# Kernel tuning notes

Hardware: AMD Instinct MI355X
Metric: run time of the kernel (lower is better)

## Reference

```python
import jax, jax.numpy as jnp
import numpy as np

D_MODEL = 1024
N_HEADS = 16
DH = D_MODEL // N_HEADS
ROPE_THETA = 10000.0


def rotate_half(u):
    h = u.shape[-1] // 2
    return jnp.concatenate([-u[..., h:], u[..., :h]], axis=-1)


def apply_rope(q, k, cos, sin):
    return q * cos + rotate_half(q) * sin, k * cos + rotate_half(k) * sin


def setup_inputs() -> dict:
    key = jax.random.key(0)
    ks = jax.random.split(key, 6)
    B, S = 2, 2048
    x = jax.random.normal(ks[0], (B, S, D_MODEL), dtype=jnp.float32)
    y = jax.random.normal(ks[1], (B, S, D_MODEL), dtype=jnp.float32)
    wq = 0.01 * jax.random.normal(ks[2], (D_MODEL, D_MODEL), dtype=jnp.float32)
    wk = 0.01 * jax.random.normal(ks[3], (D_MODEL, D_MODEL), dtype=jnp.float32)
    wv = 0.01 * jax.random.normal(ks[4], (D_MODEL, D_MODEL), dtype=jnp.float32)
    wo = 0.01 * jax.random.normal(ks[5], (D_MODEL, D_MODEL), dtype=jnp.float32)
    return {"x": x, "y": y, "wq": wq, "wk": wk, "wv": wv, "wo": wo}


def reference(x, y, wq, wk, wv, wo):
    B, S, D = x.shape
    past_length = 0  # default; kv_cache=None

    Q = x @ wq.T                      # (B,S,D)
    K = y                             # NOTE: K is y un-projected (as in source)
    V = y @ wv.T
    # K1 = x @ wk.T is computed in the source but immediately overwritten
    # by the buggy second apply_rope call -> wk is unused in the output.
    V1 = x @ wo.T

    def heads(t):
        return t.reshape(B, S, N_HEADS, DH).transpose(0, 2, 1, 3)  # (B,H,S,dh)

    q_h, k_h, v_h, v1_h = heads(Q), heads(K), heads(V), heads(V1)

    # RoPE tables (past_length:past_length+S rows of the cache)
    freqs = 1.0 / ROPE_THETA ** (jnp.arange(0, DH, 2, dtype=jnp.float32) / DH)
    emb = jnp.arange(past_length, past_length + S, dtype=jnp.float32)[:, None] * freqs[None, :]
    cos = jnp.concatenate([jnp.cos(emb), jnp.cos(emb)], axis=-1)[None, None]  # (1,1,S,dh)
    sin = jnp.concatenate([jnp.sin(emb), jnp.sin(emb)], axis=-1)[None, None]

    q_h, k_h = apply_rope(q_h, k_h, cos, sin)
    # faithful to source: k1 = rope applied AGAIN to the already-roped k
    _, k1_h = apply_rope(q_h, k_h, cos, sin)

    k_full = jnp.concatenate([k_h, k1_h], axis=2)   # (B,H,2S,dh)
    v_full = jnp.concatenate([v_h, v1_h], axis=2)
    S_full = k_full.shape[2]

    # mask: tril(diagonal=past_length) over (S,S_full), last S cols = eye(S)
    rows = jnp.arange(S)[:, None]
    cols = jnp.arange(S_full)[None, :]
    mask = cols <= rows + past_length
    mask = mask.at[:, -S:].set(jnp.eye(S, dtype=bool))  # (S,S_full)

    scores = jnp.einsum("bhqd,bhkd->bhqk", q_h, k_full) / jnp.sqrt(jnp.asarray(DH, x.dtype))
    scores = jnp.where(mask[None, None], scores, jnp.asarray(-1e30, x.dtype))
    attn = jax.nn.softmax(scores, axis=-1)
    out = jnp.einsum("bhqk,bhkd->bhqd", attn, v_full)
    out = out.transpose(0, 2, 1, 3).reshape(B, S, D)

    k_ret = k_full[:, :, :-S, :]
    return out, k_ret
```

## Files before the change

### kernel.cpp

```cpp
#include <hip/hip_runtime.h>

#define DM 1024
#define NHEADS 16
#define DHEAD 64
#define BB 2
#define SS 2048
#define BH (BB*NHEADS)

typedef __attribute__((ext_vector_type(8))) short short8;
typedef __attribute__((ext_vector_type(4))) float float4v;
typedef unsigned short ushort_t;

#define LN1E4_D32 0.28782313662425572f

static __device__ __forceinline__ unsigned short f2bf(float f) {
    union { float f; unsigned u; } v; v.f = f;
    unsigned r = v.u + 0x7fffu + ((v.u >> 16) & 1u);
    return (unsigned short)(r >> 16);
}
static __device__ __forceinline__ float bf2f(unsigned short u) {
    union { float f; unsigned u; } v; v.u = ((unsigned)u) << 16;
    return v.f;
}
static __device__ __forceinline__ unsigned cvtpk_bf16(float lo, float hi) {
    unsigned r;
    asm("v_cvt_pk_bf16_f32 %0, %1, %2" : "=v"(r) : "v"(lo), "v"(hi));
    return r;
}

static __device__ __forceinline__ void gload16(const ushort_t* g, ushort_t* l) {
    __builtin_amdgcn_global_load_lds(
        (const __attribute__((address_space(1))) void*)g,
        (__attribute__((address_space(3))) void*)l, 16, 0, 0);
}

__global__ __launch_bounds__(256) void cvt_tile_kernel(
        const float* __restrict__ x, const float* __restrict__ wq,
        const float* __restrict__ wv, const float* __restrict__ wo,
        ushort_t* __restrict__ xb, ushort_t* __restrict__ wqb,
        ushort_t* __restrict__ wvb, ushort_t* __restrict__ wob) {
    int C = blockIdx.x * 256 + threadIdx.x;
    int c  = C & 511;
    int tl = C >> 9;
    int rb = tl >> 5, kb = tl & 31;
    const float* src; ushort_t* dst; int r0;
    if (rb < 32)      { src = x;  r0 = rb * 128;        dst = xb  + (size_t)tl * 4096; }
    else if (rb < 40) { src = wq; r0 = (rb - 32) * 128; dst = wqb + (size_t)(((rb - 32) * 32) + kb) * 4096; }
    else if (rb < 48) { src = wv; r0 = (rb - 40) * 128; dst = wvb + (size_t)(((rb - 40) * 32) + kb) * 4096; }
    else              { src = wo; r0 = (rb - 48) * 128; dst = wob + (size_t)(((rb - 48) * 32) + kb) * 4096; }
    int row = c >> 2, g = c & 3;
    int kk3 = g ^ ((row >> 1) & 3);
    const float* s = src + (size_t)(r0 + row) * DM + kb * 32 + kk3 * 8;
    float4 a0 = *reinterpret_cast<const float4*>(s);
    float4 a1 = *reinterpret_cast<const float4*>(s + 4);
    short8 v;
    v[0] = (short)f2bf(a0.x); v[1] = (short)f2bf(a0.y);
    v[2] = (short)f2bf(a0.z); v[3] = (short)f2bf(a0.w);
    v[4] = (short)f2bf(a1.x); v[5] = (short)f2bf(a1.y);
    v[6] = (short)f2bf(a1.z); v[7] = (short)f2bf(a1.w);
    *reinterpret_cast<short8*>(dst + c * 8) = v;
}

__global__ __launch_bounds__(256) void rope_k_kernel(const float* __restrict__ y,
        float* __restrict__ kout, ushort_t* __restrict__ khb, ushort_t* __restrict__ yb) {
    int t = blockIdx.x * blockDim.x + threadIdx.x;
    int i8 = t & 3;
    int s  = (t >> 2) & (SS - 1);
    int bh = t >> 13;
    int h = bh & (NHEADS - 1), b = bh >> 4;

    const float* yp = y + ((size_t)(b * SS + s)) * DM + h * DHEAD + i8 * 8;
    float4 a0 = *reinterpret_cast<const float4*>(yp);
    float4 a1 = *reinterpret_cast<const float4*>(yp + 4);
    float4 b0 = *reinterpret_cast<const float4*>(yp + 32);
    float4 b1 = *reinterpret_cast<const float4*>(yp + 36);
    float u0[8] = {a0.x, a0.y, a0.z, a0.w, a1.x, a1.y, a1.z, a1.w};
    float u1[8] = {b0.x, b0.y, b0.z, b0.w, b1.x, b1.y, b1.z, b1.w};
    float lo[8], hi[8];
#pragma unroll
    for (int j = 0; j < 8; j++) {
        int i = i8 * 8 + j;
        float freq = __expf(-(float)i * LN1E4_D32);
        float th = (float)s * freq;
        float cv = cosf(th), sv = sinf(th);
        lo[j] = u0[j] * cv - u1[j] * sv;
        hi[j] = u1[j] * cv + u0[j] * sv;
    }
    float* op = kout + ((size_t)bh * SS + s) * DHEAD + i8 * 8;
    *reinterpret_cast<float4*>(op)      = (float4){lo[0], lo[1], lo[2], lo[3]};
    *reinterpret_cast<float4*>(op + 4)  = (float4){lo[4], lo[5], lo[6], lo[7]};
    *reinterpret_cast<float4*>(op + 32) = (float4){hi[0], hi[1], hi[2], hi[3]};
    *reinterpret_cast<float4*>(op + 36) = (float4){hi[4], hi[5], hi[6], hi[7]};

    ushort_t* kb = khb + ((size_t)bh * 32 + (s >> 6)) * 4096 + (s & 63) * 64;
    short8 vlo, vhi;
#pragma unroll
    for (int j = 0; j < 8; j++) { vlo[j] = (short)f2bf(lo[j]); vhi[j] = (short)f2bf(hi[j]); }
    *reinterpret_cast<short8*>(kb + ((i8 ^ (s & 7)) << 3))       = vlo;
    *reinterpret_cast<short8*>(kb + (((i8 + 4) ^ (s & 7)) << 3)) = vhi;

    int rowm = b * SS + s;
    int rowin = rowm & 127, rbm = rowm >> 7;
    int g = i8 ^ ((rowin >> 1) & 3);
    ushort_t* yt = yb + ((size_t)(rbm * 32 + h * 2)) * 4096 + rowin * 32 + (g << 3);
    short8 ulo, uhi;
#pragma unroll
    for (int j = 0; j < 8; j++) { ulo[j] = (short)f2bf(u0[j]); uhi[j] = (short)f2bf(u1[j]); }
    *reinterpret_cast<short8*>(yt)        = ulo;
    *reinterpret_cast<short8*>(yt + 4096) = uhi;
}

__global__ __launch_bounds__(256, 2) void gemm3_kernel(
        const ushort_t* __restrict__ xb, const ushort_t* __restrict__ yb,
        const ushort_t* __restrict__ wqb, const ushort_t* __restrict__ wvb,
        const ushort_t* __restrict__ wob,
        ushort_t* __restrict__ qh, ushort_t* __restrict__ vt, ushort_t* __restrict__ v1h) {
    __shared__ __align__(16) char smem[34816];
    ushort_t* As = (ushort_t*)smem;
    ushort_t* Bs = (ushort_t*)(smem + 16384);
    ushort_t (*Ct)[136] = (ushort_t(*)[136])smem;

    int bid = blockIdx.x;
    int xcd = bid & 7;
    int s_  = bid >> 3;
    int zo  = s_ >> 5;
    int z   = (zo == 0) ? 0 : (zo == 1 ? 2 : 1);
    int t_  = s_ & 31;
    int n0  = (t_ >> 2) * 128;
    int m0  = (xcd * 4 + (t_ & 3)) * 128;

    const ushort_t* A = (z == 1) ? yb : xb;
    const ushort_t* W = (z == 0) ? wqb : (z == 1 ? wvb : wob);
    ushort_t* O = (z == 0) ? qh : (z == 1 ? vt : v1h);

    const ushort_t* Atl = A + (size_t)(m0 >> 7) * 32 * 4096;
    const ushort_t* Wtl = W + (size_t)(n0 >> 7) * 32 * 4096;

    int tid = threadIdx.x;
    int wave = tid >> 6, lane = tid & 63, quad = lane >> 4, l15 = lane & 15;
    int wr = (wave >> 1) * 64, wc = (wave & 1) * 64;

    int gi0 = tid * 8, gi1 = (256 + tid) * 8;
    int li0 = (tid & 192) * 8, li1 = (256 + (tid & 192)) * 8;

    int aoff[4], boff[4];
#pragma unroll
    for (int mi = 0; mi < 4; mi++) {
        int row = wr + mi * 16 + l15;
        aoff[mi] = row * 32 + ((quad ^ ((row >> 1) & 3)) << 3);
    }
#pragma unroll
    for (int ni = 0; ni < 4; ni++) {
        int row = wc + ni * 16 + l15;
        boff[ni] = row * 32 + ((quad ^ ((row >> 1) & 3)) << 3);
    }

    float4v acc[4][4];
#pragma unroll
    for (int a = 0; a < 4; a++)
#pragma unroll
        for (int b = 0; b < 4; b++)
            acc[a][b] = (float4v){0.f, 0.f, 0.f, 0.f};

    gload16(Atl + gi0, As + li0); gload16(Atl + gi1, As + li1);
    gload16(Wtl + gi0, Bs + li0); gload16(Wtl + gi1, Bs + li1);
    int cur = 0;

    for (int kb = 0; kb < 32; kb++) {
        __syncthreads();
        if (kb + 1 < 32) {
            const ushort_t* at = Atl + (size_t)(kb + 1) * 4096;
            const ushort_t* wt = Wtl + (size_t)(kb + 1) * 4096;
            int nb = (cur ^ 1) * 4096;
            gload16(at + gi0, As + nb + li0); gload16(at + gi1, As + nb + li1);
            gload16(wt + gi0, Bs + nb + li0); gload16(wt + gi1, Bs + nb + li1);
        }
        const ushort_t* Ac = As + cur * 4096;
        const ushort_t* Bc = Bs + cur * 4096;
        short8 af[4], bfr[4];
#pragma unroll
        for (int mi = 0; mi < 4; mi++)
            af[mi] = *reinterpret_cast<const short8*>(&Ac[aoff[mi]]);
#pragma unroll
        for (int ni = 0; ni < 4; ni++)
            bfr[ni] = *reinterpret_cast<const short8*>(&Bc[boff[ni]]);
#pragma unroll
        for (int mi = 0; mi < 4; mi++)
#pragma unroll
            for (int ni = 0; ni < 4; ni++)
                acc[mi][ni] = __builtin_amdgcn_mfma_f32_16x16x32_bf16(af[mi], bfr[ni], acc[mi][ni], 0, 0, 0);
        cur ^= 1;
    }

    if (z == 0) {
#pragma unroll
        for (int mi = 0; mi < 4; mi++)
#pragma unroll
            for (int r = 0; r < 4; r++) {
                int m = m0 + wr + mi * 16 + quad * 4 + r;
                float pos = (float)(m & (SS - 1));
#pragma unroll
                for (int ni = 0; ni < 2; ni++) {
                    int d = ni * 16 + l15;
                    float f = __expf(-(float)d * LN1E4_D32);
                    float th = pos * f;
                    float cv, sv;
                    __sincosf(th, &sv, &cv);
                    float u0 = acc[mi][ni][r], u1 = acc[mi][ni + 2][r];
                    acc[mi][ni][r]     = u0 * cv - u1 * sv;
                    acc[mi][ni + 2][r] = u1 * cv + u0 * sv;
                }
            }
    }

    __syncthreads();
#pragma unroll
    for (int mi = 0; mi < 4; mi++)
#pragma unroll
        for (int ni = 0; ni < 4; ni++) {
            int col = wc + ni * 16 + l15;
#pragma unroll
            for (int r = 0; r < 4; r++)
                Ct[wr + mi * 16 + quad * 4 + r][col] = f2bf(acc[mi][ni][r]);
        }
    __syncthreads();
    int h0 = n0 >> 6;
    if (z == 1) {
        int b = m0 >> 11;
        int s0 = m0 & (SS - 1);
#pragma unroll
        for (int it = 0; it < 8; it++) {
            int c = it * 256 + tid;
            int dh  = c & 63;
            int k16 = (c >> 6) & 15;
            int hh  = c >> 10;
            short8 v;
#pragma unroll
            for (int e = 0; e < 8; e++)
                v[e] = (short)Ct[k16 * 8 + e][hh * 64 + dh];
            int kt = (s0 >> 6) + (k16 >> 3);
            size_t off = ((size_t)((b * NHEADS + h0 + hh) * 32 + kt)) * 4096
                       + dh * 64 + (((k16 & 7) ^ (dh & 7)) << 3);
            *reinterpret_cast<short8*>(&O[off]) = v;
        }
    } else {
#pragma unroll
        for (int it = 0; it < 8; it++) {
            int c = it * 256 + tid;
            int o = c >> 3, j = c & 7;
            int hh = o >> 7, mr = o & 127;
            int m = m0 + mr, b = m >> 11, si = m & (SS - 1);
            uint4 v = *reinterpret_cast<const uint4*>(&Ct[mr][hh * 64 + j * 8]);
            *reinterpret_cast<uint4*>(
                &O[((size_t)((b * NHEADS + h0 + hh) * SS + si)) * DHEAD + j * 8]) = v;
        }
    }
}

template<bool MASKED>
static __device__ __forceinline__ void attn_tile(
        const ushort_t* __restrict__ Kc, const ushort_t* __restrict__ Vc, int kbase,
        int quad, int l15, int q0w, const short8* qf,
        ushort_t* __restrict__ Psw, float4v* Oa, float& lsum) {
    float4v sa[4];
#pragma unroll
    for (int t2 = 0; t2 < 4; t2++) sa[t2] = (float4v){0.f, 0.f, 0.f, 0.f};
#pragma unroll
    for (int t2 = 0; t2 < 4; t2++) {
        int key = t2 * 16 + l15;
        int ro = key * 64, sw = key & 7;
#pragma unroll
        for (int half = 0; half < 2; half++) {
            short8 kf = *reinterpret_cast<const short8*>(&Kc[ro + (((half * 4 + quad) ^ sw) << 3)]);
            sa[t2] = __builtin_amdgcn_mfma_f32_16x16x32_bf16(kf, qf[half], sa[t2], 0, 0, 0);
        }
    }
    int query = q0w + l15;
    int swl = l15 & 7;
#pragma unroll
    for (int t2 = 0; t2 < 4; t2++) {
        float p[4];
#pragma unroll
        for (int r = 0; r < 4; r++) {
            float e = __expf(sa[t2][r] * 0.125f);
            if (MASKED) {
                int key = kbase + t2 * 16 + quad * 4 + r;
                p[r] = (key <= query) ? e : 0.f;
            } else {
                p[r] = e;
            }
        }
        lsum += (p[0] + p[1]) + (p[2] + p[3]);
        unsigned w0 = cvtpk_bf16(p[0], p[1]);
        unsigned w1 = cvtpk_bf16(p[2], p[3]);
        int chunk = (((t2 * 2 + (quad >> 1)) ^ swl) << 3) + (quad & 1) * 4;
        *reinterpret_cast<unsigned*>(&Psw[l15 * 64 + chunk])     = w0;
        *reinterpret_cast<unsigned*>(&Psw[l15 * 64 + chunk + 2]) = w1;
    }
    short8 pf0 = *reinterpret_cast<const short8*>(&Psw[l15 * 64 + ((quad ^ swl) << 3)]);
    short8 pf1 = *reinterpret_cast<const short8*>(&Psw[l15 * 64 + (((4 + quad) ^ swl) << 3)]);
#pragma unroll
    for (int t = 0; t < 4; t++) {
        int dh = t * 16 + l15;
        int ro = dh * 64, sw = dh & 7;
        short8 vf0 = *reinterpret_cast<const short8*>(&Vc[ro + ((quad ^ sw) << 3)]);
        short8 vf1 = *reinterpret_cast<const short8*>(&Vc[ro + (((4 + quad) ^ sw) << 3)]);
        Oa[t] = __builtin_amdgcn_mfma_f32_16x16x32_bf16(pf0, vf0, Oa[t], 0, 0, 0);
        Oa[t] = __builtin_amdgcn_mfma_f32_16x16x32_bf16(pf1, vf1, Oa[t], 0, 0, 0);
    }
}

__global__ __launch_bounds__(512, 2) void attn_kernel(
        const ushort_t* __restrict__ qh, const float* __restrict__ kf32,
        const ushort_t* __restrict__ khb, const ushort_t* __restrict__ vtb,
        const ushort_t* __restrict__ v1h, float* __restrict__ out) {
    __shared__ __align__(16) ushort_t Ks[2][4096];
    __shared__ __align__(16) ushort_t Vt[2][4096];
    __shared__ __align__(16) ushort_t Ps[8][16][64];
    __shared__ float sdiag[8][16];
    __shared__ float sred[8][16];

    int bid = blockIdx.x;
    int bh = (bid & 7) * 4 + ((bid >> 3) & 3);
    int jq = 15 - (bid >> 5);
    int q0 = jq * 128;

    int tid = threadIdx.x, wave = tid >> 6, lane = tid & 63, quad = lane >> 4, l15 = lane & 15;
    int q0w = q0 + wave * 16;
    const ushort_t* qp  = qh  + (size_t)bh * SS * DHEAD;
    const float*    kp  = kf32 + (size_t)bh * SS * DHEAD;
    const ushort_t* v1p = v1h + (size_t)bh * SS * DHEAD;
    const ushort_t* ktb = khb + (size_t)bh * 32 * 4096;
    const ushort_t* vtt = vtb + (size_t)bh * 32 * 4096;

    short8 qf[2];
    qf[0] = *reinterpret_cast<const short8*>(&qp[(q0w + l15) * DHEAD + quad * 8]);
    qf[1] = *reinterpret_cast<const short8*>(&qp[(q0w + l15) * DHEAD + 32 + quad * 8]);

    float4v Oa[4];
#pragma unroll
    for (int t = 0; t < 4; t++) Oa[t] = (float4v){0.f, 0.f, 0.f, 0.f};
    float lsum = 0.f;

    int gi = tid * 8;
    int li = (tid & 448) * 8;

    int ntiles = jq * 2 + 2;
    gload16(ktb + gi, &Ks[0][li]);
    gload16(vtt + gi, &Vt[0][li]);
    int cur = 0;

    for (int kt = 0; kt < ntiles; kt++) {
        __syncthreads();
        if (kt + 1 < ntiles) {
            const ushort_t* gk = ktb + (size_t)(kt + 1) * 4096;
            const ushort_t* gv = vtt + (size_t)(kt + 1) * 4096;
            int nb = cur ^ 1;
            gload16(gk + gi, &Ks[nb][li]);
            gload16(gv + gi, &Vt[nb][li]);
        }
        int kbase = kt * 64;
        if (kbase <= q0w + 15) {
            if (kbase + 63 <= q0w)
                attn_tile<false>(Ks[cur], Vt[cur], kbase, quad, l15, q0w, qf,
                                 &Ps[wave][0][0], Oa, lsum);
            else
                attn_tile<true>(Ks[cur], Vt[cur], kbase, quad, l15, q0w, qf,
                                &Ps[wave][0][0], Oa, lsum);
        }
        cur ^= 1;
    }

    lsum += __shfl_xor(lsum, 16);
    lsum += __shfl_xor(lsum, 32);
    if (quad == 0) sred[wave][l15] = lsum;

    {
        int sk = q0w + l15;
        const float* krow = kp + (size_t)sk * DHEAD;
        short8 k1lo, k1hi;
#pragma unroll
        for (int j = 0; j < 8; j++) {
            int d = quad * 8 + j;
            float f = __expf(-(float)d * LN1E4_D32);
            float th = (float)sk * f;
            float cv, sv;
            __sincosf(th, &sv, &cv);
            float a = krow[d], b2 = krow[d + 32];
            k1lo[j] = (short)f2bf(a * cv - b2 * sv);
            k1hi[j] = (short)f2bf(b2 * cv + a * sv);
        }
        float4v sd4 = (float4v){0.f, 0.f, 0.f, 0.f};
        sd4 = __builtin_amdgcn_mfma_f32_16x16x32_bf16(qf[0], k1lo, sd4, 0, 0, 0);
        sd4 = __builtin_amdgcn_mfma_f32_16x16x32_bf16(qf[1], k1hi, sd4, 0, 0, 0);
#pragma unroll
        for (int r = 0; r < 4; r++)
            if (l15 == quad * 4 + r) sdiag[wave][l15] = sd4[r] * 0.125f;
        __syncthreads();

        int b = bh >> 4, h = bh & (NHEADS - 1);
#pragma unroll
        for (int r = 0; r < 4; r++) {
            float ls = sred[wave][quad * 4 + r];
            float pd = __expf(sdiag[wave][quad * 4 + r]);
            int query = q0w + quad * 4 + r;
            float linv = 1.f / (ls + pd);
#pragma unroll
            for (int t = 0; t < 4; t++) {
                float v1v = bf2f(v1p[query * DHEAD + t * 16 + l15]);
                float o = (Oa[t][r] + pd * v1v) * linv;
                out[(b * SS + query) * DM + h * DHEAD + t * 16 + l15] = o;
            }
        }
    }
}

extern "C" void kernel_launch(void* const* d_in, const int* in_sizes, int n_in,
                              void* d_out, int out_size, void* d_ws, size_t ws_size,
                              hipStream_t stream) {
    const float* x  = (const float*)d_in[0];
    const float* y  = (const float*)d_in[1];
    const float* wq = (const float*)d_in[2];
    const float* wv = (const float*)d_in[4];
    const float* wo = (const float*)d_in[5];
    float* outp  = (float*)d_out;
    float* k_out = outp + (size_t)BB * SS * DM;

    char* ws = (char*)d_ws;
    ushort_t* vtb = (ushort_t*)(ws);
    ushort_t* v1b = (ushort_t*)(ws + (8ull  << 20));
    ushort_t* qhb = (ushort_t*)(ws + (16ull << 20));
    ushort_t* khb = (ushort_t*)(ws + (24ull << 20));
    ushort_t* xb  = (ushort_t*)(ws + (32ull << 20));
    ushort_t* yb  = (ushort_t*)(ws + (40ull << 20));
    ushort_t* wqb = (ushort_t*)(ws + (48ull << 20));
    ushort_t* wvb = (ushort_t*)(ws + (50ull << 20));
    ushort_t* wob = (ushort_t*)(ws + (52ull << 20));

    cvt_tile_kernel<<<3584, 256, 0, stream>>>(x, wq, wv, wo, xb, wqb, wvb, wob);
    rope_k_kernel<<<1024, 256, 0, stream>>>(y, k_out, khb, yb);
    gemm3_kernel<<<768, 256, 0, stream>>>(xb, yb, wqb, wvb, wob, qhb, vtb, v1b);
    attn_kernel<<<512, 512, 0, stream>>>(qhb, k_out, khb, vtb, v1b, outp);
}
```

Measured before the change: 176.0 us.

## Process 32 queries per wave in attention to reuse K/V fragments

Each wave now handles two 16-row query blocks, so every K and V fragment loaded from shared memory feeds two MFMA chains. The block shrinks to 4 waves (256 threads), each thread issues twice as many global-to-LDS loads per tile, and launch bounds change to 256 threads with 3 blocks per SM. This halves LDS reads per unit of MFMA work, but it raises register use and reduces parallelism per block. Causal masking is coarser because a wave covers 32 rows, so some extra masked tiles are computed.

```diff
diff --git a/kernel.cpp b/kernel.cpp
--- a/kernel.cpp
+++ b/kernel.cpp
@@ -258,67 +258,78 @@
 }
 
 template<bool MASKED>
-static __device__ __forceinline__ void attn_tile(
+static __device__ __forceinline__ void attn_tile32(
         const ushort_t* __restrict__ Kc, const ushort_t* __restrict__ Vc, int kbase,
-        int quad, int l15, int q0w, const short8* qf,
-        ushort_t* __restrict__ Psw, float4v* Oa, float& lsum) {
-    float4v sa[4];
-#pragma unroll
-    for (int t2 = 0; t2 < 4; t2++) sa[t2] = (float4v){0.f, 0.f, 0.f, 0.f};
+        int quad, int l15, int q0w, const short8 (*qf)[2],
+        ushort_t* __restrict__ Psw, float4v (*Oa)[4], float* lsum) {
+    float4v sa[2][4];
+#pragma unroll
+    for (int row = 0; row < 2; row++)
+#pragma unroll
+        for (int t2 = 0; t2 < 4; t2++) sa[row][t2] = (float4v){0.f, 0.f, 0.f, 0.f};
 #pragma unroll
     for (int t2 = 0; t2 < 4; t2++) {
         int key = t2 * 16 + l15;
         int ro = key * 64, sw = key & 7;
-#pragma unroll
-        for (int half = 0; half < 2; half++) {
-            short8 kf = *reinterpret_cast<const short8*>(&Kc[ro + (((half * 4 + quad) ^ sw) << 3)]);
-            sa[t2] = __builtin_amdgcn_mfma_f32_16x16x32_bf16(kf, qf[half], sa[t2], 0, 0, 0);
-        }
-    }
-    int query = q0w + l15;
+        short8 kf0 = *reinterpret_cast<const short8*>(&Kc[ro + ((quad ^ sw) << 3)]);
+        short8 kf1 = *reinterpret_cast<const short8*>(&Kc[ro + (((4 + quad) ^ sw) << 3)]);
+        sa[0][t2] = __builtin_amdgcn_mfma_f32_16x16x32_bf16(kf0, qf[0][0], sa[0][t2], 0, 0, 0);
+        sa[0][t2] = __builtin_amdgcn_mfma_f32_16x16x32_bf16(kf1, qf[0][1], sa[0][t2], 0, 0, 0);
+        sa[1][t2] = __builtin_amdgcn_mfma_f32_16x16x32_bf16(kf0, qf[1][0], sa[1][t2], 0, 0, 0);
+        sa[1][t2] = __builtin_amdgcn_mfma_f32_16x16x32_bf16(kf1, qf[1][1], sa[1][t2], 0, 0, 0);
+    }
     int swl = l15 & 7;
 #pragma unroll
-    for (int t2 = 0; t2 < 4; t2++) {
-        float p[4];
-#pragma unroll
-        for (int r = 0; r < 4; r++) {
-            float e = __expf(sa[t2][r] * 0.125f);
-            if (MASKED) {
-                int key = kbase + t2 * 16 + quad * 4 + r;
-                p[r] = (key <= query) ? e : 0.f;
-            } else {
-                p[r] = e;
+    for (int row = 0; row < 2; row++) {
+        int query = q0w + row * 16 + l15;
+#pragma unroll
+        for (int t2 = 0; t2 < 4; t2++) {
+            float p[4];
+#pragma unroll
+            for (int r = 0; r < 4; r++) {
+                float e = __expf(sa[row][t2][r] * 0.125f);
+                if (MASKED) {
+                    int key = kbase + t2 * 16 + quad * 4 + r;
+                    p[r] = (key <= query) ? e : 0.f;
+                } else {
+                    p[r] = e;
+                }
             }
-        }
-        lsum += (p[0] + p[1]) + (p[2] + p[3]);
-        unsigned w0 = cvtpk_bf16(p[0], p[1]);
-        unsigned w1 = cvtpk_bf16(p[2], p[3]);
-        int chunk = (((t2 * 2 + (quad >> 1)) ^ swl) << 3) + (quad & 1) * 4;
-        *reinterpret_cast<unsigned*>(&Psw[l15 * 64 + chunk])     = w0;
-        *reinterpret_cast<unsigned*>(&Psw[l15 * 64 + chunk + 2]) = w1;
-    }
-    short8 pf0 = *reinterpret_cast<const short8*>(&Psw[l15 * 64 + ((quad ^ swl) << 3)]);
-    short8 pf1 = *reinterpret_cast<const short8*>(&Psw[l15 * 64 + (((4 + quad) ^ swl) << 3)]);
+            lsum[row] += (p[0] + p[1]) + (p[2] + p[3]);
+            unsigned w0 = cvtpk_bf16(p[0], p[1]);
+            unsigned w1 = cvtpk_bf16(p[2], p[3]);
+            int chunk = (((t2 * 2 + (quad >> 1)) ^ swl) << 3) + (quad & 1) * 4;
+            *reinterpret_cast<unsigned*>(&Psw[(row * 16 + l15) * 64 + chunk])     = w0;
+            *reinterpret_cast<unsigned*>(&Psw[(row * 16 + l15) * 64 + chunk + 2]) = w1;
+        }
+    }
+    short8 pf[2][2];
+    pf[0][0] = *reinterpret_cast<const short8*>(&Psw[l15 * 64 + ((quad ^ swl) << 3)]);
+    pf[0][1] = *reinterpret_cast<const short8*>(&Psw[l15 * 64 + (((4 + quad) ^ swl) << 3)]);
+    pf[1][0] = *reinterpret_cast<const short8*>(&Psw[(16 + l15) * 64 + ((quad ^ swl) << 3)]);
+    pf[1][1] = *reinterpret_cast<const short8*>(&Psw[(16 + l15) * 64 + (((4 + quad) ^ swl) << 3)]);
 #pragma unroll
     for (int t = 0; t < 4; t++) {
         int dh = t * 16 + l15;
         int ro = dh * 64, sw = dh & 7;
         short8 vf0 = *reinterpret_cast<const short8*>(&Vc[ro + ((quad ^ sw) << 3)]);
         short8 vf1 = *reinterpret_cast<const short8*>(&Vc[ro + (((4 + quad) ^ sw) << 3)]);
-        Oa[t] = __builtin_amdgcn_mfma_f32_16x16x32_bf16(pf0, vf0, Oa[t], 0, 0, 0);
-        Oa[t] = __builtin_amdgcn_mfma_f32_16x16x32_bf16(pf1, vf1, Oa[t], 0, 0, 0);
-    }
-}
-
-__global__ __launch_bounds__(512, 2) void attn_kernel(
+        Oa[0][t] = __builtin_amdgcn_mfma_f32_16x16x32_bf16(pf[0][0], vf0, Oa[0][t], 0, 0, 0);
+        Oa[0][t] = __builtin_amdgcn_mfma_f32_16x16x32_bf16(pf[0][1], vf1, Oa[0][t], 0, 0, 0);
+        Oa[1][t] = __builtin_amdgcn_mfma_f32_16x16x32_bf16(pf[1][0], vf0, Oa[1][t], 0, 0, 0);
+        Oa[1][t] = __builtin_amdgcn_mfma_f32_16x16x32_bf16(pf[1][1], vf1, Oa[1][t], 0, 0, 0);
+    }
+}
+
+__global__ __launch_bounds__(256, 3) void attn_kernel(
         const ushort_t* __restrict__ qh, const float* __restrict__ kf32,
         const ushort_t* __restrict__ khb, const ushort_t* __restrict__ vtb,
         const ushort_t* __restrict__ v1h, float* __restrict__ out) {
     __shared__ __align__(16) ushort_t Ks[2][4096];
     __shared__ __align__(16) ushort_t Vt[2][4096];
-    __shared__ __align__(16) ushort_t Ps[8][16][64];
-    __shared__ float sdiag[8][16];
-    __shared__ float sred[8][16];
+    __shared__ __align__(16) ushort_t Ps[4][32][64];
+    __shared__ float sdiag[4][32];
+    __shared__ float sred[4][32];
 
     int bid = blockIdx.x;
     int bh = (bid & 7) * 4 + ((bid >> 3) & 3);
@@ -326,28 +337,34 @@
     int q0 = jq * 128;
 
     int tid = threadIdx.x, wave = tid >> 6, lane = tid & 63, quad = lane >> 4, l15 = lane & 15;
-    int q0w = q0 + wave * 16;
+    int q0w = q0 + wave * 32;
     const ushort_t* qp  = qh  + (size_t)bh * SS * DHEAD;
     const float*    kp  = kf32 + (size_t)bh * SS * DHEAD;
     const ushort_t* v1p = v1h + (size_t)bh * SS * DHEAD;
     const ushort_t* ktb = khb + (size_t)bh * 32 * 4096;
     const ushort_t* vtt = vtb + (size_t)bh * 32 * 4096;
 
-    short8 qf[2];
-    qf[0] = *reinterpret_cast<const short8*>(&qp[(q0w + l15) * DHEAD + quad * 8]);
-    qf[1] = *reinterpret_cast<const short8*>(&qp[(q0w + l15) * DHEAD + 32 + quad * 8]);
-
-    float4v Oa[4];
-#pragma unroll
-    for (int t = 0; t < 4; t++) Oa[t] = (float4v){0.f, 0.f, 0.f, 0.f};
-    float lsum = 0.f;
-
-    int gi = tid * 8;
-    int li = (tid & 448) * 8;
+    short8 qf[2][2];
+#pragma unroll
+    for (int row = 0; row < 2; row++) {
+        int q = q0w + row * 16 + l15;
+        qf[row][0] = *reinterpret_cast<const short8*>(&qp[q * DHEAD + quad * 8]);
+        qf[row][1] = *reinterpret_cast<const short8*>(&qp[q * DHEAD + 32 + quad * 8]);
+    }
+
+    float4v Oa[2][4];
+#pragma unroll
+    for (int row = 0; row < 2; row++)
+#pragma unroll
+        for (int t = 0; t < 4; t++) Oa[row][t] = (float4v){0.f, 0.f, 0.f, 0.f};
+    float lsum[2] = {0.f, 0.f};
+
+    int gi0 = tid * 8, gi1 = (256 + tid) * 8;
+    int li0 = (tid & 192) * 8, li1 = (256 + (tid & 192)) * 8;
 
     int ntiles = jq * 2 + 2;
-    gload16(ktb + gi, &Ks[0][li]);
-    gload16(vtt + gi, &Vt[0][li]);
+    gload16(ktb + gi0, &Ks[0][li0]); gload16(ktb + gi1, &Ks[0][li1]);
+    gload16(vtt + gi0, &Vt[0][li0]); gload16(vtt + gi1, &Vt[0][li1]);
     int cur = 0;
 
     for (int kt = 0; kt < ntiles; kt++) {
@@ -356,27 +373,32 @@
             const ushort_t* gk = ktb + (size_t)(kt + 1) * 4096;
             const ushort_t* gv = vtt + (size_t)(kt + 1) * 4096;
             int nb = cur ^ 1;
-            gload16(gk + gi, &Ks[nb][li]);
-            gload16(gv + gi, &Vt[nb][li]);
+            gload16(gk + gi0, &Ks[nb][li0]); gload16(gk + gi1, &Ks[nb][li1]);
+            gload16(gv + gi0, &Vt[nb][li0]); gload16(gv + gi1, &Vt[nb][li1]);
         }
         int kbase = kt * 64;
-        if (kbase <= q0w + 15) {
+        if (kbase <= q0w + 31) {
             if (kbase + 63 <= q0w)
-                attn_tile<false>(Ks[cur], Vt[cur], kbase, quad, l15, q0w, qf,
-                                 &Ps[wave][0][0], Oa, lsum);
+                attn_tile32<false>(Ks[cur], Vt[cur], kbase, quad, l15, q0w, qf,
+                                   &Ps[wave][0][0], Oa, lsum);
             else
-                attn_tile<true>(Ks[cur], Vt[cur], kbase, quad, l15, q0w, qf,
-                                &Ps[wave][0][0], Oa, lsum);
+                attn_tile32<true>(Ks[cur], Vt[cur], kbase, quad, l15, q0w, qf,
+                                  &Ps[wave][0][0], Oa, lsum);
         }
         cur ^= 1;
     }
 
-    lsum += __shfl_xor(lsum, 16);
-    lsum += __shfl_xor(lsum, 32);
-    if (quad == 0) sred[wave][l15] = lsum;
-
-    {
-        int sk = q0w + l15;
+#pragma unroll
+    for (int row = 0; row < 2; row++) {
+        float ls = lsum[row];
+        ls += __shfl_xor(ls, 16);
+        ls += __shfl_xor(ls, 32);
+        if (quad == row) sred[wave][row * 16 + l15] = ls;
+    }
+
+#pragma unroll
+    for (int row = 0; row < 2; row++) {
+        int sk = q0w + row * 16 + l15;
         const float* krow = kp + (size_t)sk * DHEAD;
         short8 k1lo, k1hi;
 #pragma unroll
@@ -391,24 +413,27 @@
             k1hi[j] = (short)f2bf(b2 * cv + a * sv);
         }
         float4v sd4 = (float4v){0.f, 0.f, 0.f, 0.f};
-        sd4 = __builtin_amdgcn_mfma_f32_16x16x32_bf16(qf[0], k1lo, sd4, 0, 0, 0);
-        sd4 = __builtin_amdgcn_mfma_f32_16x16x32_bf16(qf[1], k1hi, sd4, 0, 0, 0);
+        sd4 = __builtin_amdgcn_mfma_f32_16x16x32_bf16(qf[row][0], k1lo, sd4, 0, 0, 0);
+        sd4 = __builtin_amdgcn_mfma_f32_16x16x32_bf16(qf[row][1], k1hi, sd4, 0, 0, 0);
 #pragma unroll
         for (int r = 0; r < 4; r++)
-            if (l15 == quad * 4 + r) sdiag[wave][l15] = sd4[r] * 0.125f;
-        __syncthreads();
-
-        int b = bh >> 4, h = bh & (NHEADS - 1);
+            if (l15 == quad * 4 + r) sdiag[wave][row * 16 + l15] = sd4[r] * 0.125f;
+    }
+    __syncthreads();
+
+    int b = bh >> 4, h = bh & (NHEADS - 1);
+#pragma unroll
+    for (int row = 0; row < 2; row++) {
 #pragma unroll
         for (int r = 0; r < 4; r++) {
-            float ls = sred[wave][quad * 4 + r];
-            float pd = __expf(sdiag[wave][quad * 4 + r]);
-            int query = q0w + quad * 4 + r;
+            float ls = sred[wave][row * 16 + quad * 4 + r];
+            float pd = __expf(sdiag[wave][row * 16 + quad * 4 + r]);
+            int query = q0w + row * 16 + quad * 4 + r;
             float linv = 1.f / (ls + pd);
 #pragma unroll
             for (int t = 0; t < 4; t++) {
                 float v1v = bf2f(v1p[query * DHEAD + t * 16 + l15]);
-                float o = (Oa[t][r] + pd * v1v) * linv;
+                float o = (Oa[row][t][r] + pd * v1v) * linv;
                 out[(b * SS + query) * DM + h * DHEAD + t * 16 + l15] = o;
             }
         }
@@ -440,5 +465,5 @@
     cvt_tile_kernel<<<3584, 256, 0, stream>>>(x, wq, wv, wo, xb, wqb, wvb, wob);
     rope_k_kernel<<<1024, 256, 0, stream>>>(y, k_out, khb, yb);
     gemm3_kernel<<<768, 256, 0, stream>>>(xb, yb, wqb, wvb, wob, qhb, vtb, v1b);
-    attn_kernel<<<512, 512, 0, stream>>>(qhb, k_out, khb, vtb, v1b, outp);
-}
+    attn_kernel<<<512, 256, 0, stream>>>(qhb, k_out, khb, vtb, v1b, outp);
+}
```

Result: no change. 177.8 us (+1.0%).
